# Optimization experiments

Measured on AMD Instinct MI355X. Metric: run time of the kernel, lower is better.

Reference implementation:

```python
import jax, jax.numpy as jnp
import numpy as np
import math

HIDDEN = 2048
N_HEADS = 16
HEAD = HIDDEN // N_HEADS
B, S = 2, 2048


def setup_inputs() -> dict:
    key = jax.random.key(0)
    k1, k2, k3 = jax.random.split(key, 3)
    scale = 1.0 / math.sqrt(HIDDEN)
    return {
        "x": jax.random.normal(k1, (B, S, HIDDEN), dtype=jnp.float32),
        "w_qkv": jax.random.normal(k2, (HIDDEN, 3 * HIDDEN), dtype=jnp.float32) * scale,
        "b_qkv": jnp.zeros((3 * HIDDEN,), dtype=jnp.float32),
        "w_out": jax.random.normal(k3, (HIDDEN, HIDDEN), dtype=jnp.float32) * scale,
        "b_out": jnp.zeros((HIDDEN,), dtype=jnp.float32),
    }


def reference(x, w_qkv, b_qkv, w_out, b_out):
    b, s, _ = x.shape
    qkv = x @ w_qkv + b_qkv                      # [b, s, 3*hidden]
    q, k, v = jnp.split(qkv, 3, axis=-1)
    # 'b n (h l) -> b h n l'
    def heads(t):
        return t.reshape(b, s, N_HEADS, HEAD).transpose(0, 2, 1, 3)
    q, k, v = heads(q), heads(k), heads(v)
    scores = jnp.einsum("bhql,bhkl->bhqk", q, k) / math.sqrt(HEAD)
    # causal mask: positions where q_ind < k_ind get -10000 (matches source)
    q_ind = jnp.arange(s)[:, None]
    k_ind = jnp.arange(s)[None, :]
    scores = jnp.where(q_ind < k_ind, jnp.float32(-10000.0), scores)
    probs = jax.nn.softmax(scores, axis=-1)
    combined = jnp.einsum("bhqk,bhkl->bhql", probs, v)
    # 'b h q l -> b q (h l)'
    combined = combined.transpose(0, 2, 1, 3).reshape(b, s, HIDDEN)
    return combined @ w_out + b_out
```

## Files before the change

kernel.cpp:

```cpp
#include <hip/hip_runtime.h>
#include <hip/hip_bf16.h>

typedef __attribute__((ext_vector_type(4))) float f32x4;
typedef __attribute__((ext_vector_type(16))) float f32x16;
typedef __attribute__((ext_vector_type(8))) short bf16x8;

#define GBL_AS(p) (const __attribute__((address_space(1))) void*)(p)
#define LDS_AS(p) (__attribute__((address_space(3))) void*)(p)

__device__ __forceinline__ void gload_lds16(const void* g, void* l) {
  __builtin_amdgcn_global_load_lds(GBL_AS(g), LDS_AS(l), 16, 0, 0);
}

__device__ __forceinline__ ushort f2bf(float f) {
  union { float f; unsigned int u; } v; v.f = f;
  unsigned int r = v.u + 0x7fffu + ((v.u >> 16) & 1u);
  return (ushort)(r >> 16);
}

__global__ void cast_f32_bf16_kernel(const float4* __restrict__ in,
                                     ushort4* __restrict__ out, int n4) {
  int i = blockIdx.x * 256 + threadIdx.x;
  if (i < n4) {
    float4 v = in[i];
    ushort4 o;
    o.x = f2bf(v.x); o.y = f2bf(v.y); o.z = f2bf(v.z); o.w = f2bf(v.w);
    out[i] = o;
  }
}

__global__ void transpose_cast_kernel(const float* __restrict__ in,
                                      ushort* __restrict__ out, int R, int C) {
  __shared__ float tile[64][65];
  int tx = threadIdx.x & 63, ty = threadIdx.x >> 6;
  int r0 = blockIdx.y * 64, c0 = blockIdx.x * 64;
#pragma unroll
  for (int i = 0; i < 64; i += 4)
    tile[ty + i][tx] = in[(size_t)(r0 + ty + i) * C + (c0 + tx)];
  __syncthreads();
#pragma unroll
  for (int i = 0; i < 64; i += 4)
    out[(size_t)(c0 + ty + i) * R + (r0 + tx)] = f2bf(tile[tx][ty + i]);
}

template <int MODE>
__global__ __launch_bounds__(256, 2) void gemm_bt_kernel(
    const ushort* __restrict__ A, const ushort* __restrict__ Bt,
    const float* __restrict__ bias, float* __restrict__ C,
    ushort* __restrict__ Qo, ushort* __restrict__ Ko, ushort* __restrict__ Vo,
    int M, int N, int K) {
  __shared__ ushort As[128 * 64];
  __shared__ ushort Bs[128 * 64];
  const int tid = threadIdx.x;
  const int w = tid >> 6, l = tid & 63;
  const int wr = w >> 1, wc = w & 1;
  const int m0 = blockIdx.y * 128, n0 = blockIdx.x * 128;

  f32x4 acc[4][4] = {};

  const int lr = l >> 3;
  const int lc = (l & 7) ^ lr;

  for (int k0 = 0; k0 < K; k0 += 64) {
#pragma unroll
    for (int i = 0; i < 4; ++i) {
      int row = i * 32 + w * 8 + lr;
      gload_lds16(A + (size_t)(m0 + row) * K + k0 + lc * 8,
                  (char*)As + (i * 32 + w * 8) * 128);
      gload_lds16(Bt + (size_t)(n0 + row) * K + k0 + lc * 8,
                  (char*)Bs + (i * 32 + w * 8) * 128);
    }
    __syncthreads();
    const char* Ab = (const char*)As;
    const char* Bb = (const char*)Bs;
#pragma unroll
    for (int ks = 0; ks < 2; ++ks) {
      bf16x8 af[4], bfr[4];
      int cc = ks * 4 + (l >> 4);
#pragma unroll
      for (int mi = 0; mi < 4; ++mi) {
        int row = wr * 64 + mi * 16 + (l & 15);
        af[mi] = *(const bf16x8*)(Ab + row * 128 + ((cc ^ (row & 7)) << 4));
      }
#pragma unroll
      for (int ni = 0; ni < 4; ++ni) {
        int row = wc * 64 + ni * 16 + (l & 15);
        bfr[ni] = *(const bf16x8*)(Bb + row * 128 + ((cc ^ (row & 7)) << 4));
      }
#pragma unroll
      for (int mi = 0; mi < 4; ++mi)
#pragma unroll
        for (int ni = 0; ni < 4; ++ni)
          acc[mi][ni] = __builtin_amdgcn_mfma_f32_16x16x32_bf16(
              af[mi], bfr[ni], acc[mi][ni], 0, 0, 0);
    }
    __syncthreads();
  }

  if (MODE == 0) {
#pragma unroll
    for (int mi = 0; mi < 4; ++mi) {
      int row = m0 + wr * 64 + mi * 16 + ((l >> 4) << 2);
#pragma unroll
      for (int ni = 0; ni < 4; ++ni) {
        int col = n0 + wc * 64 + ni * 16 + (l & 15);
        float b = bias[col];
#pragma unroll
        for (int r = 0; r < 4; ++r)
          C[(size_t)(row + r) * N + col] = acc[mi][ni][r] + b;
      }
    }
  } else {
    const float qscale = 0.08838834764831845f * 1.4426950408889634f;
#pragma unroll
    for (int ni = 0; ni < 4; ++ni) {
      int n = n0 + wc * 64 + ni * 16 + (l & 15);
      int which = n >> 11;
      int cc2 = n & 2047;
      int h = cc2 >> 7, d = cc2 & 127;
      float b = bias[n];
#pragma unroll
      for (int mi = 0; mi < 4; ++mi) {
        int m = m0 + wr * 64 + mi * 16 + ((l >> 4) << 2);
        int bb = m >> 11, s = m & 2047;
        int bh = bb * 16 + h;
        if (which == 0) {
#pragma unroll
          for (int r = 0; r < 4; ++r)
            Qo[((size_t)bh * 2048 + s + r) * 128 + d] =
                f2bf((acc[mi][ni][r] + b) * qscale);
        } else if (which == 1) {
#pragma unroll
          for (int r = 0; r < 4; ++r)
            Ko[((size_t)bh * 2048 + s + r) * 128 + d] = f2bf(acc[mi][ni][r] + b);
        } else {
          ushort4 pk;
          pk.x = f2bf(acc[mi][ni][0] + b);
          pk.y = f2bf(acc[mi][ni][1] + b);
          pk.z = f2bf(acc[mi][ni][2] + b);
          pk.w = f2bf(acc[mi][ni][3] + b);
          *(ushort4*)(Vo + ((size_t)bh * 128 + d) * 2048 + s) = pk;
        }
      }
    }
  }
}

__global__ __launch_bounds__(512, 2) void attn_kernel(
    const ushort* __restrict__ Qg, const ushort* __restrict__ Kg,
    const ushort* __restrict__ Vtg, ushort* __restrict__ Og) {
  constexpr int S = 2048, D = 128;
  __shared__ ushort Kl[2][64 * 128];
  __shared__ ushort Vl[2][128 * 64];

  const int tid = threadIdx.x, w = tid >> 6, l = tid & 63;
  const int lid = blockIdx.x;
  const int bh = lid & 31;
  const int j = lid >> 5;
  const int g = w >> 2, wv = w & 3;
  const int qb = (g == 0) ? (8 + j) : (7 - j);
  const int wq0 = qb * 128 + wv * 32;
  const int nt_blk = 18 + 2 * j;
  const int ql = l & 31, h32 = l >> 5;

  const ushort* Qb = Qg + (size_t)bh * S * D;
  const ushort* Kb = Kg + (size_t)bh * S * D;
  const ushort* Vb = Vtg + (size_t)bh * D * S;

  bf16x8 qf[8];
#pragma unroll
  for (int ks = 0; ks < 8; ++ks)
    qf[ks] = *(const bf16x8*)(Qb + (size_t)(wq0 + ql) * D + ks * 16 + h32 * 8);

  f32x16 o[4];
#pragma unroll
  for (int dt = 0; dt < 4; ++dt) o[dt] = 0.f;
  float mrun = -1e30f, lrun = 0.f;

  auto stage = [&](int t, int buf) {
    const int k0 = t * 64;
#pragma unroll
    for (int s2 = 0; s2 < 2; ++s2) {
      int i = w * 2 + s2;
      int row = i * 4 + (l >> 4);
      int ck = (l & 15) ^ (row & 7);
      gload_lds16(Kb + (size_t)(k0 + row) * D + ck * 8,
                  (char*)Kl[buf] + i * 1024);
    }
#pragma unroll
    for (int s2 = 0; s2 < 2; ++s2) {
      int i = w * 2 + s2;
      int row = i * 8 + (l >> 3);
      int ck = (l & 7) ^ (row & 7);
      gload_lds16(Vb + (size_t)row * S + k0 + ck * 8,
                  (char*)Vl[buf] + i * 1024);
    }
  };

  stage(0, 0);

  for (int t = 0; t < nt_blk; ++t) {
    const int cur = t & 1;
    const int k0 = t * 64;
    if (t + 1 < nt_blk) {
      stage(t + 1, cur ^ 1);
      asm volatile("s_waitcnt vmcnt(4)" ::: "memory");
    } else {
      asm volatile("s_waitcnt vmcnt(0)" ::: "memory");
    }
    __builtin_amdgcn_s_barrier();

    if (k0 < wq0 + 32) {
      const char* Kc = (const char*)Kl[cur];
      const char* Vc = (const char*)Vl[cur];

      bf16x8 kf0[8], kf1[8];
      {
        const int swz0 = ql & 7;
        const char* base0 = Kc + ql * 256;
        const char* base1 = Kc + (32 + ql) * 256;
#pragma unroll
        for (int ks = 0; ks < 8; ++ks) {
          int c = 2 * ks + h32;
          kf0[ks] = *(const bf16x8*)(base0 + ((c ^ swz0) << 4));
          kf1[ks] = *(const bf16x8*)(base1 + ((c ^ swz0) << 4));
        }
      }
      f32x16 sa[2];
      sa[0] = 0.f; sa[1] = 0.f;
      __builtin_amdgcn_s_setprio(1);
#pragma unroll
      for (int ks = 0; ks < 8; ++ks) {
        sa[0] = __builtin_amdgcn_mfma_f32_32x32x16_bf16(kf0[ks], qf[ks], sa[0],
                                                        0, 0, 0);
        sa[1] = __builtin_amdgcn_mfma_f32_32x32x16_bf16(kf1[ks], qf[ks], sa[1],
                                                        0, 0, 0);
      }
      __builtin_amdgcn_s_setprio(0);

      if (k0 + 63 > wq0) {
        int qq = wq0 + ql;
#pragma unroll
        for (int kt = 0; kt < 2; ++kt) {
          int kb = k0 + kt * 32 + 4 * h32;
#pragma unroll
          for (int rr = 0; rr < 16; ++rr) {
            int kk = kb + (rr & 3) + 8 * (rr >> 2);
            if (qq < kk) sa[kt][rr] = -1e9f;
          }
        }
      }

      float tmax = -1e30f;
#pragma unroll
      for (int kt = 0; kt < 2; ++kt)
#pragma unroll
        for (int rr = 0; rr < 16; ++rr) tmax = fmaxf(tmax, sa[kt][rr]);
      tmax = fmaxf(tmax, __shfl_xor(tmax, 32));

      if (!__all(tmax <= mrun + 11.5f)) {
        float mnew = fmaxf(mrun, tmax);
        float e = __builtin_amdgcn_exp2f(mrun - mnew);
        lrun *= e;
        mrun = mnew;
#pragma unroll
        for (int dt = 0; dt < 4; ++dt) o[dt] *= e;
      }

      float rsum = 0.f;
#pragma unroll
      for (int kt = 0; kt < 2; ++kt)
#pragma unroll
        for (int rr = 0; rr < 16; ++rr) {
          float p = __builtin_amdgcn_exp2f(sa[kt][rr] - mrun);
          sa[kt][rr] = p;
          rsum += p;
        }
      rsum += __shfl_xor(rsum, 32);
      lrun += rsum;

#pragma unroll
      for (int kt = 0; kt < 2; ++kt) {
#pragma unroll
        for (int u = 0; u < 2; ++u) {
          int c = 4 * kt + 2 * u + h32;
          bf16x8 vf[4];
#pragma unroll
          for (int dt = 0; dt < 4; ++dt) {
            int row = dt * 32 + ql;
            vf[dt] = *(const bf16x8*)(Vc + row * 128 + ((c ^ (row & 7)) << 4));
          }
          int A0, B0, A1, B1;
          asm("v_cvt_pk_bf16_f32 %0, %1, %2"
              : "=v"(A0) : "v"(sa[kt][u * 8 + 0]), "v"(sa[kt][u * 8 + 1]));
          asm("v_cvt_pk_bf16_f32 %0, %1, %2"
              : "=v"(B0) : "v"(sa[kt][u * 8 + 2]), "v"(sa[kt][u * 8 + 3]));
          asm("v_cvt_pk_bf16_f32 %0, %1, %2"
              : "=v"(A1) : "v"(sa[kt][u * 8 + 4]), "v"(sa[kt][u * 8 + 5]));
          asm("v_cvt_pk_bf16_f32 %0, %1, %2"
              : "=v"(B1) : "v"(sa[kt][u * 8 + 6]), "v"(sa[kt][u * 8 + 7]));
          auto r02 = __builtin_amdgcn_permlane32_swap(A0, A1, false, false);
          auto r13 = __builtin_amdgcn_permlane32_swap(B0, B1, false, false);
          union { int i[4]; bf16x8 v; } pu;
          pu.i[0] = r02[0];
          pu.i[1] = r13[0];
          pu.i[2] = r02[1];
          pu.i[3] = r13[1];
          __builtin_amdgcn_s_setprio(1);
#pragma unroll
          for (int dt = 0; dt < 4; ++dt)
            o[dt] = __builtin_amdgcn_mfma_f32_32x32x16_bf16(vf[dt], pu.v, o[dt],
                                                            0, 0, 0);
          __builtin_amdgcn_s_setprio(0);
        }
      }
    }
    asm volatile("s_waitcnt lgkmcnt(0)" ::: "memory");
    __builtin_amdgcn_s_barrier();
  }

  const int b = bh >> 4, h = bh & 15;
  float inv = 1.0f / lrun;
  size_t rowbase = ((size_t)b * 2048 + (wq0 + ql)) * 2048 + h * 128;
#pragma unroll
  for (int dt = 0; dt < 4; ++dt)
#pragma unroll
    for (int r4 = 0; r4 < 4; ++r4) {
      int col = dt * 32 + r4 * 8 + h32 * 4;
      ushort4 pk;
      pk.x = f2bf(o[dt][r4 * 4 + 0] * inv);
      pk.y = f2bf(o[dt][r4 * 4 + 1] * inv);
      pk.z = f2bf(o[dt][r4 * 4 + 2] * inv);
      pk.w = f2bf(o[dt][r4 * 4 + 3] * inv);
      *(ushort4*)(Og + rowbase + col) = pk;
    }
}

extern "C" void kernel_launch(void* const* d_in, const int* in_sizes, int n_in,
                              void* d_out, int out_size, void* d_ws,
                              size_t ws_size, hipStream_t stream) {
  const float* x = (const float*)d_in[0];
  const float* w_qkv = (const float*)d_in[1];
  const float* b_qkv = (const float*)d_in[2];
  const float* w_out = (const float*)d_in[3];
  const float* b_out = (const float*)d_in[4];
  float* out = (float*)d_out;
  char* ws = (char*)d_ws;

  if (ws_size < 92274688u) return;
  ushort* xb = (ushort*)(ws);
  ushort* wqkvt = (ushort*)(ws + 16777216);
  ushort* Q = (ushort*)(ws + 41943040);
  ushort* Kb = (ushort*)(ws + 58720256);
  ushort* Vt = (ushort*)(ws + 75497472);
  ushort* comb = xb;
  ushort* woutt = wqkvt;

  cast_f32_bf16_kernel<<<8192, 256, 0, stream>>>((const float4*)x, (ushort4*)xb,
                                                 2097152);
  transpose_cast_kernel<<<dim3(96, 32), 256, 0, stream>>>(w_qkv, wqkvt, 2048,
                                                          6144);
  gemm_bt_kernel<1><<<dim3(48, 32), 256, 0, stream>>>(
      xb, wqkvt, b_qkv, nullptr, Q, Kb, Vt, 4096, 6144, 2048);
  transpose_cast_kernel<<<dim3(32, 32), 256, 0, stream>>>(w_out, woutt, 2048,
                                                          2048);
  attn_kernel<<<dim3(256), 512, 0, stream>>>(Q, Kb, Vt, comb);
  gemm_bt_kernel<0><<<dim3(16, 32), 256, 0, stream>>>(
      comb, woutt, b_out, out, nullptr, nullptr, nullptr, 4096, 2048, 2048);
}
```

Measured before the change: 230.4 us.

## Split long causal query blocks across KV halves with a merge kernel

The attention launch changes from 256 blocks of 512 threads, each pairing two query blocks, to 768 blocks of 256 threads, each handling one 128-row query block. Query blocks in the upper half of the sequence are split into two KV-range halves. Each half writes unnormalized bf16 partial outputs plus its row max and sum into scratch space in the output buffer, and a new merge kernel combines them with rescaling. The goal is more, smaller blocks to balance causal work across CUs. The cost is an extra launch, extra scratch traffic and bf16 rounding of the partial outputs.

```diff
diff --git a/kernel.cpp b/kernel.cpp
--- a/kernel.cpp
+++ b/kernel.cpp
@@ -16,6 +16,11 @@
   union { float f; unsigned int u; } v; v.f = f;
   unsigned int r = v.u + 0x7fffu + ((v.u >> 16) & 1u);
   return (ushort)(r >> 16);
+}
+
+__device__ __forceinline__ float bf2f(ushort u) {
+  union { unsigned int u; float f; } v; v.u = ((unsigned int)u) << 16;
+  return v.f;
 }
 
 __global__ void cast_f32_bf16_kernel(const float4* __restrict__ in,
@@ -146,9 +151,11 @@
   }
 }
 
-__global__ __launch_bounds__(512, 2) void attn_kernel(
+#define PART_STRIDE 34304
+__global__ __launch_bounds__(256, 2) void attn_kernel(
     const ushort* __restrict__ Qg, const ushort* __restrict__ Kg,
-    const ushort* __restrict__ Vtg, ushort* __restrict__ Og) {
+    const ushort* __restrict__ Vtg, ushort* __restrict__ Og,
+    char* __restrict__ part) {
   constexpr int S = 2048, D = 128;
   __shared__ ushort Kl[2][64 * 128];
   __shared__ ushort Vl[2][128 * 64];
@@ -156,11 +163,17 @@
   const int tid = threadIdx.x, w = tid >> 6, l = tid & 63;
   const int lid = blockIdx.x;
   const int bh = lid & 31;
-  const int j = lid >> 5;
-  const int g = w >> 2, wv = w & 3;
-  const int qb = (g == 0) ? (8 + j) : (7 - j);
-  const int wq0 = qb * 128 + wv * 32;
-  const int nt_blk = 18 + 2 * j;
+  const int u = lid >> 5;
+  int qb, t0, nt, h;
+  bool split;
+  if (u < 8) { qb = u; t0 = 0; nt = 2 * u + 2; h = 0; split = false; }
+  else {
+    int v = u - 8;
+    qb = 8 + (v >> 1); h = v & 1;
+    nt = qb + 1; t0 = h * (qb + 1);
+    split = true;
+  }
+  const int wq0 = qb * 128 + w * 32;
   const int ql = l & 31, h32 = l >> 5;
 
   const ushort* Qb = Qg + (size_t)bh * S * D;
@@ -180,16 +193,16 @@
   auto stage = [&](int t, int buf) {
     const int k0 = t * 64;
 #pragma unroll
-    for (int s2 = 0; s2 < 2; ++s2) {
-      int i = w * 2 + s2;
+    for (int s2 = 0; s2 < 4; ++s2) {
+      int i = w * 4 + s2;
       int row = i * 4 + (l >> 4);
       int ck = (l & 15) ^ (row & 7);
       gload_lds16(Kb + (size_t)(k0 + row) * D + ck * 8,
                   (char*)Kl[buf] + i * 1024);
     }
 #pragma unroll
-    for (int s2 = 0; s2 < 2; ++s2) {
-      int i = w * 2 + s2;
+    for (int s2 = 0; s2 < 4; ++s2) {
+      int i = w * 4 + s2;
       int row = i * 8 + (l >> 3);
       int ck = (l & 7) ^ (row & 7);
       gload_lds16(Vb + (size_t)row * S + k0 + ck * 8,
@@ -197,14 +210,14 @@
     }
   };
 
-  stage(0, 0);
-
-  for (int t = 0; t < nt_blk; ++t) {
-    const int cur = t & 1;
-    const int k0 = t * 64;
-    if (t + 1 < nt_blk) {
-      stage(t + 1, cur ^ 1);
-      asm volatile("s_waitcnt vmcnt(4)" ::: "memory");
+  stage(t0, 0);
+
+  for (int tt = 0; tt < nt; ++tt) {
+    const int cur = tt & 1;
+    const int k0 = (t0 + tt) * 64;
+    if (tt + 1 < nt) {
+      stage(t0 + tt + 1, cur ^ 1);
+      asm volatile("s_waitcnt vmcnt(8)" ::: "memory");
     } else {
       asm volatile("s_waitcnt vmcnt(0)" ::: "memory");
     }
@@ -282,8 +295,8 @@
 #pragma unroll
       for (int kt = 0; kt < 2; ++kt) {
 #pragma unroll
-        for (int u = 0; u < 2; ++u) {
-          int c = 4 * kt + 2 * u + h32;
+        for (int u2 = 0; u2 < 2; ++u2) {
+          int c = 4 * kt + 2 * u2 + h32;
           bf16x8 vf[4];
 #pragma unroll
           for (int dt = 0; dt < 4; ++dt) {
@@ -292,13 +305,13 @@
           }
           int A0, B0, A1, B1;
           asm("v_cvt_pk_bf16_f32 %0, %1, %2"
-              : "=v"(A0) : "v"(sa[kt][u * 8 + 0]), "v"(sa[kt][u * 8 + 1]));
+              : "=v"(A0) : "v"(sa[kt][u2 * 8 + 0]), "v"(sa[kt][u2 * 8 + 1]));
           asm("v_cvt_pk_bf16_f32 %0, %1, %2"
-              : "=v"(B0) : "v"(sa[kt][u * 8 + 2]), "v"(sa[kt][u * 8 + 3]));
+              : "=v"(B0) : "v"(sa[kt][u2 * 8 + 2]), "v"(sa[kt][u2 * 8 + 3]));
           asm("v_cvt_pk_bf16_f32 %0, %1, %2"
-              : "=v"(A1) : "v"(sa[kt][u * 8 + 4]), "v"(sa[kt][u * 8 + 5]));
+              : "=v"(A1) : "v"(sa[kt][u2 * 8 + 4]), "v"(sa[kt][u2 * 8 + 5]));
           asm("v_cvt_pk_bf16_f32 %0, %1, %2"
-              : "=v"(B1) : "v"(sa[kt][u * 8 + 6]), "v"(sa[kt][u * 8 + 7]));
+              : "=v"(B1) : "v"(sa[kt][u2 * 8 + 6]), "v"(sa[kt][u2 * 8 + 7]));
           auto r02 = __builtin_amdgcn_permlane32_swap(A0, A1, false, false);
           auto r13 = __builtin_amdgcn_permlane32_swap(B0, B1, false, false);
           union { int i[4]; bf16x8 v; } pu;
@@ -319,21 +332,78 @@
     __builtin_amdgcn_s_barrier();
   }
 
-  const int b = bh >> 4, h = bh & 15;
-  float inv = 1.0f / lrun;
-  size_t rowbase = ((size_t)b * 2048 + (wq0 + ql)) * 2048 + h * 128;
-#pragma unroll
-  for (int dt = 0; dt < 4; ++dt)
-#pragma unroll
-    for (int r4 = 0; r4 < 4; ++r4) {
-      int col = dt * 32 + r4 * 8 + h32 * 4;
-      ushort4 pk;
-      pk.x = f2bf(o[dt][r4 * 4 + 0] * inv);
-      pk.y = f2bf(o[dt][r4 * 4 + 1] * inv);
-      pk.z = f2bf(o[dt][r4 * 4 + 2] * inv);
-      pk.w = f2bf(o[dt][r4 * 4 + 3] * inv);
-      *(ushort4*)(Og + rowbase + col) = pk;
-    }
+  if (!split) {
+    const int b = bh >> 4, hh = bh & 15;
+    float inv = 1.0f / lrun;
+    size_t rowbase = ((size_t)b * 2048 + (wq0 + ql)) * 2048 + hh * 128;
+#pragma unroll
+    for (int dt = 0; dt < 4; ++dt)
+#pragma unroll
+      for (int r4 = 0; r4 < 4; ++r4) {
+        int col = dt * 32 + r4 * 8 + h32 * 4;
+        ushort4 pk;
+        pk.x = f2bf(o[dt][r4 * 4 + 0] * inv);
+        pk.y = f2bf(o[dt][r4 * 4 + 1] * inv);
+        pk.z = f2bf(o[dt][r4 * 4 + 2] * inv);
+        pk.w = f2bf(o[dt][r4 * 4 + 3] * inv);
+        *(ushort4*)(Og + rowbase + col) = pk;
+      }
+  } else {
+    const int pu_idx = ((bh * 8 + (qb - 8)) * 2 + h);
+    char* base = part + (size_t)pu_idx * PART_STRIDE;
+    const int r = w * 32 + ql;
+    if (h32 == 0) {
+      ((float*)(base + 32768))[r] = mrun;
+      ((float*)(base + 33280))[r] = lrun;
+    }
+#pragma unroll
+    for (int dt = 0; dt < 4; ++dt)
+#pragma unroll
+      for (int r4 = 0; r4 < 4; ++r4) {
+        int col = dt * 32 + r4 * 8 + h32 * 4;
+        ushort4 pk;
+        pk.x = f2bf(o[dt][r4 * 4 + 0]);
+        pk.y = f2bf(o[dt][r4 * 4 + 1]);
+        pk.z = f2bf(o[dt][r4 * 4 + 2]);
+        pk.w = f2bf(o[dt][r4 * 4 + 3]);
+        *(ushort4*)(base + r * 256 + col * 2) = pk;
+      }
+  }
+}
+
+__global__ void attn_merge_kernel(const char* __restrict__ part,
+                                  ushort* __restrict__ Og) {
+  const int blk = blockIdx.x;
+  const int bh = blk >> 3, qb = 8 + (blk & 7);
+  const char* p0 = part + (size_t)(blk * 2 + 0) * PART_STRIDE;
+  const char* p1 = part + (size_t)(blk * 2 + 1) * PART_STRIDE;
+  const int t = threadIdx.x;
+  const int r = t >> 1, cpart = t & 1;
+  float m0 = ((const float*)(p0 + 32768))[r];
+  float l0 = ((const float*)(p0 + 33280))[r];
+  float m1 = ((const float*)(p1 + 32768))[r];
+  float l1 = ((const float*)(p1 + 33280))[r];
+  float M = fmaxf(m0, m1);
+  float w0 = __builtin_amdgcn_exp2f(m0 - M);
+  float w1 = __builtin_amdgcn_exp2f(m1 - M);
+  float inv = 1.0f / (l0 * w0 + l1 * w1);
+  w0 *= inv; w1 *= inv;
+  const int b = bh >> 4, hh = bh & 15;
+  const int s = qb * 128 + r;
+  size_t obase = ((size_t)b * 2048 + s) * 2048 + hh * 128 + cpart * 64;
+  const ushort* O0 = (const ushort*)p0 + r * 128 + cpart * 64;
+  const ushort* O1 = (const ushort*)p1 + r * 128 + cpart * 64;
+#pragma unroll
+  for (int i = 0; i < 64; i += 4) {
+    ushort4 a = *(const ushort4*)(O0 + i);
+    ushort4 c = *(const ushort4*)(O1 + i);
+    ushort4 pk;
+    pk.x = f2bf(bf2f(a.x) * w0 + bf2f(c.x) * w1);
+    pk.y = f2bf(bf2f(a.y) * w0 + bf2f(c.y) * w1);
+    pk.z = f2bf(bf2f(a.z) * w0 + bf2f(c.z) * w1);
+    pk.w = f2bf(bf2f(a.w) * w0 + bf2f(c.w) * w1);
+    *(ushort4*)(Og + obase + i) = pk;
+  }
 }
 
 extern "C" void kernel_launch(void* const* d_in, const int* in_sizes, int n_in,
@@ -355,6 +425,7 @@
   ushort* Vt = (ushort*)(ws + 75497472);
   ushort* comb = xb;
   ushort* woutt = wqkvt;
+  char* part = (char*)d_out;
 
   cast_f32_bf16_kernel<<<8192, 256, 0, stream>>>((const float4*)x, (ushort4*)xb,
                                                  2097152);
@@ -364,7 +435,8 @@
       xb, wqkvt, b_qkv, nullptr, Q, Kb, Vt, 4096, 6144, 2048);
   transpose_cast_kernel<<<dim3(32, 32), 256, 0, stream>>>(w_out, woutt, 2048,
                                                           2048);
-  attn_kernel<<<dim3(256), 512, 0, stream>>>(Q, Kb, Vt, comb);
+  attn_kernel<<<dim3(768), 256, 0, stream>>>(Q, Kb, Vt, comb, part);
+  attn_merge_kernel<<<dim3(256), 256, 0, stream>>>(part, comb);
   gemm_bt_kernel<0><<<dim3(16, 32), 256, 0, stream>>>(
       comb, woutt, b_out, out, nullptr, nullptr, nullptr, 4096, 2048, 2048);
 }
```

Result: slower. 240.1 us (+4.2%).

## Load V fragments directly from global memory instead of staging in LDS

Applied to the files above, without the earlier changes.

Drops the double-buffered LDS staging of the transposed V tile. Each wave now loads its V fragments straight from global memory into registers right after the QK^T MFMAs, and the vmcnt wait is adjusted to match. This halves LDS usage and removes the LDS write/read traffic for V. In exchange, each wave issues uncoalesced-ish 16-byte global loads that duplicate V reads across the 8 waves, which adds global/L2 traffic, register pressure (32 bf16x8 registers held live) and exposed latency before the PV MFMAs.

```diff
diff --git a/kernel.cpp b/kernel.cpp
--- a/kernel.cpp
+++ b/kernel.cpp
@@ -151,7 +151,6 @@
     const ushort* __restrict__ Vtg, ushort* __restrict__ Og) {
   constexpr int S = 2048, D = 128;
   __shared__ ushort Kl[2][64 * 128];
-  __shared__ ushort Vl[2][128 * 64];
 
   const int tid = threadIdx.x, w = tid >> 6, l = tid & 63;
   const int lid = blockIdx.x;
@@ -187,14 +186,6 @@
       gload_lds16(Kb + (size_t)(k0 + row) * D + ck * 8,
                   (char*)Kl[buf] + i * 1024);
     }
-#pragma unroll
-    for (int s2 = 0; s2 < 2; ++s2) {
-      int i = w * 2 + s2;
-      int row = i * 8 + (l >> 3);
-      int ck = (l & 7) ^ (row & 7);
-      gload_lds16(Vb + (size_t)row * S + k0 + ck * 8,
-                  (char*)Vl[buf] + i * 1024);
-    }
   };
 
   stage(0, 0);
@@ -204,7 +195,7 @@
     const int k0 = t * 64;
     if (t + 1 < nt_blk) {
       stage(t + 1, cur ^ 1);
-      asm volatile("s_waitcnt vmcnt(4)" ::: "memory");
+      asm volatile("s_waitcnt vmcnt(2)" ::: "memory");
     } else {
       asm volatile("s_waitcnt vmcnt(0)" ::: "memory");
     }
@@ -212,7 +203,6 @@
 
     if (k0 < wq0 + 32) {
       const char* Kc = (const char*)Kl[cur];
-      const char* Vc = (const char*)Vl[cur];
 
       bf16x8 kf0[8], kf1[8];
       {
@@ -238,6 +228,21 @@
       }
       __builtin_amdgcn_s_setprio(0);
 
+      bf16x8 vf[2][2][4];
+      {
+        const ushort* vrow = Vb + (size_t)ql * S + k0;
+#pragma unroll
+        for (int kt = 0; kt < 2; ++kt)
+#pragma unroll
+          for (int u2 = 0; u2 < 2; ++u2) {
+            int c = 4 * kt + 2 * u2 + h32;
+#pragma unroll
+            for (int dt = 0; dt < 4; ++dt)
+              vf[kt][u2][dt] =
+                  *(const bf16x8*)(vrow + (size_t)dt * 32 * S + c * 8);
+          }
+      }
+
       if (k0 + 63 > wq0) {
         int qq = wq0 + ql;
 #pragma unroll
@@ -282,23 +287,16 @@
 #pragma unroll
       for (int kt = 0; kt < 2; ++kt) {
 #pragma unroll
-        for (int u = 0; u < 2; ++u) {
-          int c = 4 * kt + 2 * u + h32;
-          bf16x8 vf[4];
-#pragma unroll
-          for (int dt = 0; dt < 4; ++dt) {
-            int row = dt * 32 + ql;
-            vf[dt] = *(const bf16x8*)(Vc + row * 128 + ((c ^ (row & 7)) << 4));
-          }
+        for (int u2 = 0; u2 < 2; ++u2) {
           int A0, B0, A1, B1;
           asm("v_cvt_pk_bf16_f32 %0, %1, %2"
-              : "=v"(A0) : "v"(sa[kt][u * 8 + 0]), "v"(sa[kt][u * 8 + 1]));
+              : "=v"(A0) : "v"(sa[kt][u2 * 8 + 0]), "v"(sa[kt][u2 * 8 + 1]));
           asm("v_cvt_pk_bf16_f32 %0, %1, %2"
-              : "=v"(B0) : "v"(sa[kt][u * 8 + 2]), "v"(sa[kt][u * 8 + 3]));
+              : "=v"(B0) : "v"(sa[kt][u2 * 8 + 2]), "v"(sa[kt][u2 * 8 + 3]));
           asm("v_cvt_pk_bf16_f32 %0, %1, %2"
-              : "=v"(A1) : "v"(sa[kt][u * 8 + 4]), "v"(sa[kt][u * 8 + 5]));
+              : "=v"(A1) : "v"(sa[kt][u2 * 8 + 4]), "v"(sa[kt][u2 * 8 + 5]));
           asm("v_cvt_pk_bf16_f32 %0, %1, %2"
-              : "=v"(B1) : "v"(sa[kt][u * 8 + 6]), "v"(sa[kt][u * 8 + 7]));
+              : "=v"(B1) : "v"(sa[kt][u2 * 8 + 6]), "v"(sa[kt][u2 * 8 + 7]));
           auto r02 = __builtin_amdgcn_permlane32_swap(A0, A1, false, false);
           auto r13 = __builtin_amdgcn_permlane32_swap(B0, B1, false, false);
           union { int i[4]; bf16x8 v; } pu;
@@ -309,8 +307,8 @@
           __builtin_amdgcn_s_setprio(1);
 #pragma unroll
           for (int dt = 0; dt < 4; ++dt)
-            o[dt] = __builtin_amdgcn_mfma_f32_32x32x16_bf16(vf[dt], pu.v, o[dt],
-                                                            0, 0, 0);
+            o[dt] = __builtin_amdgcn_mfma_f32_32x32x16_bf16(
+                vf[kt][u2][dt], pu.v, o[dt], 0, 0, 0);
           __builtin_amdgcn_s_setprio(0);
         }
       }
```

After: 261.2 us. 1.13x slower.
